# Kernel tuning notes

Hardware: AMD Instinct MI355X
Metric: run time of the kernel (lower is better)

Reference implementation:

```python
import jax, jax.numpy as jnp
import numpy as np

STRIDE = 2

def _conv(x, w, stride, pad):
    # NCHW input, OIHW weight
    return jax.lax.conv_general_dilated(
        x, w,
        window_strides=(stride, stride),
        padding=((pad, pad), (pad, pad)),
        dimension_numbers=("NCHW", "OIHW", "NCHW"),
    )

def setup_inputs() -> dict:
    key = jax.random.key(0)
    k1, k2, k3, k4 = jax.random.split(key, 4)
    x = jax.random.normal(k1, (64, 128, 56, 56), dtype=jnp.float32)
    w1 = jax.random.normal(k2, (256, 128, 3, 3), dtype=jnp.float32)
    w2 = jax.random.normal(k3, (256, 256, 3, 3), dtype=jnp.float32)
    w_sc = jax.random.normal(k4, (256, 128, 1, 1), dtype=jnp.float32)
    return {"x": x, "w1": w1, "w2": w2, "w_sc": w_sc}

def reference(x, w1, w2, w_sc):
    # shortcut: 1x1 binary conv, stride 2 (in_channels != out_channels / stride != 1)
    identity = _conv(x, jnp.sign(w_sc), STRIDE, 0)
    # conv1: 3x3 binary conv, stride 2, pad 1
    out = _conv(x, jnp.sign(w1), STRIDE, 1)
    out = jnp.sign(out)
    # conv2: 3x3 binary conv, stride 1, pad 1
    out = _conv(out, jnp.sign(w2), 1, 1)
    out = out + identity
    return jnp.sign(out)
```

## Files before the change

kernel.cpp:

```cpp
#include <hip/hip_runtime.h>
#include <cstdint>

#define N_IMG 64
#define IC1   128
#define HWI   56
#define OCN   256
#define HWO   28
#define PX_PER_IMG (HWO*HWO)

typedef float  f32x4_t  __attribute__((ext_vector_type(4)));
typedef __bf16 bf16x8_t __attribute__((ext_vector_type(8)));

__device__ __forceinline__ float fsign(float v) {
    return v > 0.f ? 1.f : (v < 0.f ? -1.f : 0.f);
}
__device__ __forceinline__ unsigned short bsign_bits(float v) {
    return v > 0.f ? (unsigned short)0x3F80 : (v < 0.f ? (unsigned short)0xBF80 : (unsigned short)0);
}

__global__ void transform_weights(const float* __restrict__ w1,
                                  const float* __restrict__ w2,
                                  const float* __restrict__ wsc,
                                  float* __restrict__ W1t,
                                  float* __restrict__ Wsct,
                                  unsigned short* __restrict__ W2t) {
    int idx = blockIdx.x * 256 + threadIdx.x;
    if (idx < 128*9*256) {
        int oc = idx & 255; int rest = idx >> 8;
        int kidx = rest % 9; int ic = rest / 9;
        float v = fsign(w1[(oc*IC1 + ic)*9 + kidx]);
        W1t[(((oc >> 6)*IC1 + ic)*9 + kidx)*64 + (oc & 63)] = v;
    }
    idx -= 128*9*256;
    if (idx >= 0 && idx < 128*256) {
        int oc = idx & 255; int ic = idx >> 8;
        Wsct[((oc >> 6)*IC1 + ic)*64 + (oc & 63)] = fsign(wsc[oc*IC1 + ic]);
    }
    idx -= 128*256;
    if (idx >= 0 && idx < 9*256*256) {
        int ic = idx & 255; int rest = idx >> 8;
        int oc = rest & 255; int kidx = rest >> 8;
        W2t[idx] = bsign_bits(w2[(oc*OCN + ic)*9 + kidx]);
    }
}

__global__ __launch_bounds__(256, 2) void convA(const float* __restrict__ x,
                                                const float* __restrict__ W1t,
                                                const float* __restrict__ Wsct,
                                                unsigned short* __restrict__ S,
                                                float* __restrict__ I) {
    __shared__ float Xs[8*5*64];

    const int t      = threadIdx.x;
    const int ocb    = blockIdx.x;
    const int oc0    = ocb * 64;
    const int ytile  = blockIdx.y;
    const int n      = blockIdx.z;
    const int tid_oc = t & 63;
    const int u      = t >> 6;
    const int tid_r  = u >> 1;
    const int h      = u & 1;

    float acc[14], accid[14];
    #pragma unroll
    for (int p = 0; p < 14; ++p) { acc[p] = 0.f; accid[p] = 0.f; }

    const int s_col = t & 63;
    const int s_icw = (t >> 6) * 2;
    const int s_ix  = s_col - 1;

    for (int ic0 = 0; ic0 < IC1; ic0 += 8) {
        __syncthreads();
        #pragma unroll
        for (int r = 0; r < 5; ++r) {
            int iy = 4*ytile - 1 + r;
            #pragma unroll
            for (int j = 0; j < 2; ++j) {
                int ic = s_icw + j;
                float v = 0.f;
                if ((unsigned)iy < (unsigned)HWI && (unsigned)s_ix < (unsigned)HWI)
                    v = x[((size_t)(n*IC1 + ic0 + ic)*HWI + iy)*HWI + s_ix];
                Xs[(ic*5 + r)*64 + s_col] = v;
            }
        }
        __syncthreads();

        const float* __restrict__ wp   = W1t  + ((size_t)(ocb*IC1 + ic0)*9)*64 + tid_oc;
        const float* __restrict__ wscp = Wsct + (size_t)(ocb*IC1 + ic0)*64 + tid_oc;

        for (int ic = 0; ic < 8; ++ic) {
            float w[9];
            #pragma unroll
            for (int k = 0; k < 9; ++k) w[k] = wp[(ic*9 + k)*64];
            const float wsc = wscp[ic*64];
            const float* xb = &Xs[(ic*5 + 2*tid_r)*64 + 28*h];

            #pragma unroll
            for (int ky = 0; ky < 3; ++ky) {
                float xv[32];
                const float4* rp = (const float4*)(xb + ky*64);
                #pragma unroll
                for (int i = 0; i < 8; ++i) *(float4*)&xv[i*4] = rp[i];
                #pragma unroll
                for (int kx = 0; kx < 3; ++kx) {
                    float wv = w[ky*3 + kx];
                    #pragma unroll
                    for (int p = 0; p < 14; ++p)
                        acc[p] = __builtin_fmaf(xv[2*p + kx], wv, acc[p]);
                }
                if (ky == 1) {
                    #pragma unroll
                    for (int p = 0; p < 14; ++p)
                        accid[p] = __builtin_fmaf(xv[2*p + 1], wsc, accid[p]);
                }
            }
        }
    }

    const int oy = ytile*2 + tid_r;
    #pragma unroll
    for (int p = 0; p < 14; ++p) {
        int ox = h*14 + p;
        size_t sidx = (((size_t)n*HWO + oy)*HWO + ox)*OCN + oc0 + tid_oc;
        S[sidx] = bsign_bits(acc[p]);
        I[sidx] = accid[p];
    }
}

#define SPAD 40
__global__ __launch_bounds__(256, 2) void convB(const unsigned short* __restrict__ S,
                                                const unsigned short* __restrict__ W2t,
                                                const float* __restrict__ I,
                                                float* __restrict__ out) {
    __shared__ unsigned short As[256*SPAD];
    __shared__ unsigned short Bs[64*SPAD];

    const int t    = threadIdx.x;
    const int lane = t & 63;
    const int wave = t >> 6;
    const int px0  = blockIdx.x * 64;

    f32x4_t acc[4][4];
    #pragma unroll
    for (int mi = 0; mi < 4; ++mi)
        #pragma unroll
        for (int ni = 0; ni < 4; ++ni)
            acc[mi][ni] = (f32x4_t)0.f;

    const int b_px  = t >> 2;
    const int b_icg = t & 3;
    const int pxg   = px0 + b_px;
    const int nb    = pxg / PX_PER_IMG;
    const int prb   = pxg % PX_PER_IMG;
    const int oyb   = prb / HWO;
    const int oxb   = prb % HWO;

    for (int ic0 = 0; ic0 < OCN; ic0 += 32) {
        for (int kidx = 0; kidx < 9; ++kidx) {
            const int ky = kidx / 3, kx = kidx % 3;
            __syncthreads();
            #pragma unroll
            for (int i = 0; i < 4; ++i) {
                int uu = t + 256*i;
                int oc = uu >> 2, icgl = uu & 3;
                uint4 v = *(const uint4*)&W2t[(kidx*OCN + oc)*OCN + ic0 + icgl*8];
                *(uint4*)&As[oc*SPAD + icgl*8] = v;
            }
            {
                int sy = oyb + ky - 1, sx = oxb + kx - 1;
                uint4 v = make_uint4(0u, 0u, 0u, 0u);
                if (sy >= 0 && sy < HWO && sx >= 0 && sx < HWO)
                    v = *(const uint4*)&S[((nb*HWO + sy)*HWO + sx)*OCN + ic0 + b_icg*8];
                *(uint4*)&Bs[b_px*SPAD + b_icg*8] = v;
            }
            __syncthreads();
            bf16x8_t a[4], b[4];
            #pragma unroll
            for (int mi = 0; mi < 4; ++mi) {
                int oc = wave*64 + mi*16 + (lane & 15);
                a[mi] = __builtin_bit_cast(bf16x8_t, *(const uint4*)&As[oc*SPAD + (lane >> 4)*8]);
            }
            #pragma unroll
            for (int ni = 0; ni < 4; ++ni) {
                int px = ni*16 + (lane & 15);
                b[ni] = __builtin_bit_cast(bf16x8_t, *(const uint4*)&Bs[px*SPAD + (lane >> 4)*8]);
            }
            #pragma unroll
            for (int mi = 0; mi < 4; ++mi)
                #pragma unroll
                for (int ni = 0; ni < 4; ++ni)
                    acc[mi][ni] = __builtin_amdgcn_mfma_f32_16x16x32_bf16(a[mi], b[ni], acc[mi][ni], 0, 0, 0);
        }
    }

    #pragma unroll
    for (int ni = 0; ni < 4; ++ni) {
        int px = px0 + ni*16 + (lane & 15);
        int n  = px / PX_PER_IMG;
        int pr = px % PX_PER_IMG;
        int oy = pr / HWO, ox = pr % HWO;
        #pragma unroll
        for (int mi = 0; mi < 4; ++mi) {
            int oc = wave*64 + mi*16 + (lane >> 4)*4;
            f32x4_t idv = *(const f32x4_t*)&I[(size_t)px*OCN + oc];
            #pragma unroll
            for (int r = 0; r < 4; ++r) {
                float v = acc[mi][ni][r] + idv[r];
                out[((size_t)(n*OCN + oc + r)*HWO + oy)*HWO + ox] = fsign(v);
            }
        }
    }
}

extern "C" void kernel_launch(void* const* d_in, const int* in_sizes, int n_in,
                              void* d_out, int out_size, void* d_ws, size_t ws_size,
                              hipStream_t stream) {
    (void)in_sizes; (void)n_in; (void)out_size; (void)ws_size;
    const float* x   = (const float*)d_in[0];
    const float* w1  = (const float*)d_in[1];
    const float* w2  = (const float*)d_in[2];
    const float* wsc = (const float*)d_in[3];
    float* out = (float*)d_out;

    char* ws = (char*)d_ws;
    unsigned short* S    = (unsigned short*)(ws);
    float*          I    = (float*)(ws + 25690112u);
    float*          W1t  = (float*)(ws + 77070336u);
    float*          Wsct = (float*)(ws + 78249984u);
    unsigned short* W2t  = (unsigned short*)(ws + 78381056u);

    hipLaunchKernelGGL(transform_weights, dim3(3584), dim3(256), 0, stream,
                       w1, w2, wsc, W1t, Wsct, W2t);
    hipLaunchKernelGGL(convA, dim3(4, 14, 64), dim3(256), 0, stream,
                       x, W1t, Wsct, S, I);
    hipLaunchKernelGGL(convB, dim3(784), dim3(256), 0, stream,
                       S, W2t, I, out);
}
```

Baseline: 895.9 us.

## Compute 128 output channels per convA block and stage weights in LDS

convA now computes two 64-channel groups per thread, so each block covers 128 output channels and the grid's x dimension halves. Each input tile loaded into shared memory is therefore reused across twice as many channels. The conv1 and shortcut weights for each 8-channel chunk are also staged cooperatively in shared memory instead of being read per thread from global memory, with the weight transform re-laid out to match. The cost is double the accumulator registers (56 floats) at launch bounds (256,2), more shared memory, and fewer blocks in flight.

```diff
diff --git a/kernel.cpp b/kernel.cpp
--- a/kernel.cpp
+++ b/kernel.cpp
@@ -21,22 +21,29 @@
 __global__ void transform_weights(const float* __restrict__ w1,
                                   const float* __restrict__ w2,
                                   const float* __restrict__ wsc,
-                                  float* __restrict__ W1t,
-                                  float* __restrict__ Wsct,
+                                  float* __restrict__ W1t2,
+                                  float* __restrict__ Wsct2,
                                   unsigned short* __restrict__ W2t) {
     int idx = blockIdx.x * 256 + threadIdx.x;
-    if (idx < 128*9*256) {
-        int oc = idx & 255; int rest = idx >> 8;
-        int kidx = rest % 9; int ic = rest / 9;
-        float v = fsign(w1[(oc*IC1 + ic)*9 + kidx]);
-        W1t[(((oc >> 6)*IC1 + ic)*9 + kidx)*64 + (oc & 63)] = v;
-    }
-    idx -= 128*9*256;
-    if (idx >= 0 && idx < 128*256) {
-        int oc = idx & 255; int ic = idx >> 8;
-        Wsct[((oc >> 6)*IC1 + ic)*64 + (oc & 63)] = fsign(wsc[oc*IC1 + ic]);
-    }
-    idx -= 128*256;
+    if (idx < 2*128*9*128) {
+        int oc128 = idx & 127;
+        int rest  = idx >> 7;
+        int k     = rest % 9;
+        int icc   = rest / 9;
+        int ic    = icc & 127;
+        int ocb   = icc >> 7;
+        int oc_g  = ocb*128 + oc128;
+        W1t2[idx] = fsign(w1[(oc_g*IC1 + ic)*9 + k]);
+    }
+    idx -= 2*128*9*128;
+    if (idx >= 0 && idx < 2*128*128) {
+        int oc128 = idx & 127;
+        int ic    = (idx >> 7) & 127;
+        int ocb   = idx >> 14;
+        int oc_g  = ocb*128 + oc128;
+        Wsct2[idx] = fsign(wsc[oc_g*IC1 + ic]);
+    }
+    idx -= 2*128*128;
     if (idx >= 0 && idx < 9*256*256) {
         int ic = idx & 255; int rest = idx >> 8;
         int oc = rest & 255; int kidx = rest >> 8;
@@ -45,15 +52,16 @@
 }
 
 __global__ __launch_bounds__(256, 2) void convA(const float* __restrict__ x,
-                                                const float* __restrict__ W1t,
-                                                const float* __restrict__ Wsct,
+                                                const float* __restrict__ W1t2,
+                                                const float* __restrict__ Wsct2,
                                                 unsigned short* __restrict__ S,
                                                 float* __restrict__ I) {
     __shared__ float Xs[8*5*64];
+    __shared__ float Ws[8*9*128];
+    __shared__ float Wss[8*128];
 
     const int t      = threadIdx.x;
     const int ocb    = blockIdx.x;
-    const int oc0    = ocb * 64;
     const int ytile  = blockIdx.y;
     const int n      = blockIdx.z;
     const int tid_oc = t & 63;
@@ -61,15 +69,18 @@
     const int tid_r  = u >> 1;
     const int h      = u & 1;
 
-    float acc[14], accid[14];
-    #pragma unroll
-    for (int p = 0; p < 14; ++p) { acc[p] = 0.f; accid[p] = 0.f; }
+    float acc[2][14], accid[2][14];
+    #pragma unroll
+    for (int o = 0; o < 2; ++o)
+        #pragma unroll
+        for (int p = 0; p < 14; ++p) { acc[o][p] = 0.f; accid[o][p] = 0.f; }
 
     const int s_col = t & 63;
     const int s_icw = (t >> 6) * 2;
     const int s_ix  = s_col - 1;
 
-    for (int ic0 = 0; ic0 < IC1; ic0 += 8) {
+    for (int chunk = 0; chunk < 16; ++chunk) {
+        const int ic0 = chunk * 8;
         __syncthreads();
         #pragma unroll
         for (int r = 0; r < 5; ++r) {
@@ -83,17 +94,22 @@
                 Xs[(ic*5 + r)*64 + s_col] = v;
             }
         }
+        {
+            const float4* src = (const float4*)(W1t2 + (size_t)(ocb*IC1 + ic0)*9*128);
+            #pragma unroll
+            for (int i = 0; i < 9; ++i) {
+                int li = i*256 + t;
+                *(float4*)&Ws[li*4] = src[li];
+            }
+            const float4* src2 = (const float4*)(Wsct2 + (size_t)(ocb*IC1 + ic0)*128);
+            *(float4*)&Wss[t*4] = src2[t];
+        }
         __syncthreads();
 
-        const float* __restrict__ wp   = W1t  + ((size_t)(ocb*IC1 + ic0)*9)*64 + tid_oc;
-        const float* __restrict__ wscp = Wsct + (size_t)(ocb*IC1 + ic0)*64 + tid_oc;
-
         for (int ic = 0; ic < 8; ++ic) {
-            float w[9];
-            #pragma unroll
-            for (int k = 0; k < 9; ++k) w[k] = wp[(ic*9 + k)*64];
-            const float wsc = wscp[ic*64];
             const float* xb = &Xs[(ic*5 + 2*tid_r)*64 + 28*h];
+            const float wsc0 = Wss[ic*128 + tid_oc];
+            const float wsc1 = Wss[ic*128 + 64 + tid_oc];
 
             #pragma unroll
             for (int ky = 0; ky < 3; ++ky) {
@@ -103,15 +119,22 @@
                 for (int i = 0; i < 8; ++i) *(float4*)&xv[i*4] = rp[i];
                 #pragma unroll
                 for (int kx = 0; kx < 3; ++kx) {
-                    float wv = w[ky*3 + kx];
-                    #pragma unroll
-                    for (int p = 0; p < 14; ++p)
-                        acc[p] = __builtin_fmaf(xv[2*p + kx], wv, acc[p]);
+                    const float w0 = Ws[(ic*9 + ky*3 + kx)*128 + tid_oc];
+                    const float w1v = Ws[(ic*9 + ky*3 + kx)*128 + 64 + tid_oc];
+                    #pragma unroll
+                    for (int p = 0; p < 14; ++p)
+                        acc[0][p] = __builtin_fmaf(xv[2*p + kx], w0, acc[0][p]);
+                    #pragma unroll
+                    for (int p = 0; p < 14; ++p)
+                        acc[1][p] = __builtin_fmaf(xv[2*p + kx], w1v, acc[1][p]);
                 }
                 if (ky == 1) {
                     #pragma unroll
                     for (int p = 0; p < 14; ++p)
-                        accid[p] = __builtin_fmaf(xv[2*p + 1], wsc, accid[p]);
+                        accid[0][p] = __builtin_fmaf(xv[2*p + 1], wsc0, accid[0][p]);
+                    #pragma unroll
+                    for (int p = 0; p < 14; ++p)
+                        accid[1][p] = __builtin_fmaf(xv[2*p + 1], wsc1, accid[1][p]);
                 }
             }
         }
@@ -119,11 +142,14 @@
 
     const int oy = ytile*2 + tid_r;
     #pragma unroll
-    for (int p = 0; p < 14; ++p) {
-        int ox = h*14 + p;
-        size_t sidx = (((size_t)n*HWO + oy)*HWO + ox)*OCN + oc0 + tid_oc;
-        S[sidx] = bsign_bits(acc[p]);
-        I[sidx] = accid[p];
+    for (int o = 0; o < 2; ++o) {
+        #pragma unroll
+        for (int p = 0; p < 14; ++p) {
+            int ox = h*14 + p;
+            size_t sidx = (((size_t)n*HWO + oy)*HWO + ox)*OCN + ocb*128 + o*64 + tid_oc;
+            S[sidx] = bsign_bits(acc[o][p]);
+            I[sidx] = accid[o][p];
+        }
     }
 }
 
@@ -223,16 +249,16 @@
     float* out = (float*)d_out;
 
     char* ws = (char*)d_ws;
-    unsigned short* S    = (unsigned short*)(ws);
-    float*          I    = (float*)(ws + 25690112u);
-    float*          W1t  = (float*)(ws + 77070336u);
-    float*          Wsct = (float*)(ws + 78249984u);
-    unsigned short* W2t  = (unsigned short*)(ws + 78381056u);
+    unsigned short* S     = (unsigned short*)(ws);
+    float*          I     = (float*)(ws + 25690112u);
+    float*          W1t2  = (float*)(ws + 77070336u);
+    float*          Wsct2 = (float*)(ws + 78249984u);
+    unsigned short* W2t   = (unsigned short*)(ws + 78381056u);
 
     hipLaunchKernelGGL(transform_weights, dim3(3584), dim3(256), 0, stream,
-                       w1, w2, wsc, W1t, Wsct, W2t);
-    hipLaunchKernelGGL(convA, dim3(4, 14, 64), dim3(256), 0, stream,
-                       x, W1t, Wsct, S, I);
+                       w1, w2, wsc, W1t2, Wsct2, W2t);
+    hipLaunchKernelGGL(convA, dim3(2, 14, 64), dim3(256), 0, stream,
+                       x, W1t2, Wsct2, S, I);
     hipLaunchKernelGGL(convB, dim3(784), dim3(256), 0, stream,
                        S, W2t, I, out);
 }
```

Result: faster. 838.3 us (-6.4%).
